# Optimization experiments

Hardware: AMD Instinct MI355X
Metric: run time of the kernel (lower is better)

## Reference

```python
import jax, jax.numpy as jnp
import numpy as np

N_QUBITS = 10
LAYERS = 4


def _ry(theta):
    c = jnp.cos(theta / 2).astype(jnp.complex64)
    s = jnp.sin(theta / 2).astype(jnp.complex64)
    return jnp.array([[c, -s], [s, c]], dtype=jnp.complex64)


def _rot(phi, theta, omega):
    # Rot = RZ(omega) RY(theta) RZ(phi)  (PennyLane convention)
    c = jnp.cos(theta / 2)
    s = jnp.sin(theta / 2)
    e_mm = jnp.exp(-0.5j * (phi + omega))
    e_pm = jnp.exp(0.5j * (phi - omega))
    e_mp = jnp.exp(-0.5j * (phi - omega))
    e_pp = jnp.exp(0.5j * (phi + omega))
    return jnp.array([[e_mm * c, -e_pm * s], [e_mp * s, e_pp * c]], dtype=jnp.complex64)


def _apply_1q(state, U, q):
    # state: (2,)*n complex; contract qubit axis q with 2x2 gate
    s = jnp.tensordot(U, state, axes=[[1], [q]])
    return jnp.moveaxis(s, 0, q)


def _apply_cnot(state, c, t):
    s = jnp.moveaxis(state, (c, t), (0, 1))
    s = jnp.stack([s[0], s[1, ::-1]], axis=0)
    return jnp.moveaxis(s, (0, 1), (c, t))


def _circuit(angles, weights):
    # angles: (n_qubits,) float32, weights: (layers, n_qubits, 3) float32
    n = N_QUBITS
    state = jnp.zeros((2 ** n,), dtype=jnp.complex64).at[0].set(1.0).reshape((2,) * n)
    for q in range(n):  # RY angle embedding
        state = _apply_1q(state, _ry(angles[q]), q)
    for l in range(LAYERS):  # strongly-entangling layers
        for q in range(n):
            state = _apply_1q(state, _rot(weights[l, q, 0], weights[l, q, 1], weights[l, q, 2]), q)
        for q in range(n):  # CNOT ring
            state = _apply_cnot(state, q, (q + 1) % n)
    probs = state.real ** 2 + state.imag ** 2  # (2,)*n
    zexp = []
    for q in range(n):
        p = probs.sum(axis=tuple(a for a in range(n) if a != q))
        zexp.append(p[0] - p[1])
    return jnp.stack(zexp)  # (n_qubits,)


def setup_inputs() -> dict:
    key = jax.random.key(0)
    ks = jax.random.split(key, 6)
    B, D = 8192, 784
    return {
        "x": jax.random.normal(ks[0], (B, D), dtype=jnp.float32),
        "Wp": jax.random.normal(ks[1], (N_QUBITS, D), dtype=jnp.float32) * (1.0 / np.sqrt(D)),
        "bp": jax.random.normal(ks[2], (N_QUBITS,), dtype=jnp.float32) * 0.01,
        "q_weights": jax.random.normal(ks[3], (LAYERS, N_QUBITS, 3), dtype=jnp.float32) * 0.01,
        "Wo": jax.random.normal(ks[4], (10, N_QUBITS), dtype=jnp.float32) * (1.0 / np.sqrt(N_QUBITS)),
        "bo": jax.random.normal(ks[5], (10,), dtype=jnp.float32) * 0.01,
    }


def reference(x, Wp, bp, q_weights, Wo, bo):
    # input projection + tanh
    h = jnp.tanh(x @ Wp.T + bp)  # (B, n_qubits)
    # batched quantum circuit (vmapped statevector simulation)
    q_out = jax.vmap(_circuit, in_axes=(0, None))(h, q_weights)  # (B, n_qubits)
    return q_out @ Wo.T + bo  # (B, 10) logits
```

## Files before the change

kernel.cpp:

```cpp
#include <hip/hip_runtime.h>

#define NQ      10
#define NLAYERS 4
#define D_IN    784
#define BLOCK   256

typedef __attribute__((ext_vector_type(2))) float f2;

__device__ __forceinline__ f2 swapc(f2 v) { return __builtin_shufflevector(v, v, 1, 0); }

template<int LB>
__device__ __forceinline__ float lx(float v) {
    if constexpr (LB == 1) {
        return __int_as_float(__builtin_amdgcn_update_dpp(
            0, __float_as_int(v), 0xB1, 0xF, 0xF, false));
    } else if constexpr (LB == 2) {
        return __int_as_float(__builtin_amdgcn_update_dpp(
            0, __float_as_int(v), 0x4E, 0xF, 0xF, false));
    } else if constexpr (LB == 8) {
        return __int_as_float(__builtin_amdgcn_update_dpp(
            0, __float_as_int(v), 0x128, 0xF, 0xF, false));
    } else {
        return __shfl_xor(v, LB, 64);
    }
}

template<int LB>
__device__ __forceinline__ f2 lx2(f2 v) {
    f2 r; r.x = lx<LB>(v.x); r.y = lx<LB>(v.y); return r;
}

template<int HALF>
__device__ __forceinline__ void plswap(f2 &d, f2 &s) {
    if constexpr (HALF == 32) {
        auto rx = __builtin_amdgcn_permlane32_swap(__float_as_int(d.x), __float_as_int(s.x), false, false);
        auto ry = __builtin_amdgcn_permlane32_swap(__float_as_int(d.y), __float_as_int(s.y), false, false);
        d.x = __int_as_float(rx[0]); s.x = __int_as_float(rx[1]);
        d.y = __int_as_float(ry[0]); s.y = __int_as_float(ry[1]);
    } else {
        auto rx = __builtin_amdgcn_permlane16_swap(__float_as_int(d.x), __float_as_int(s.x), false, false);
        auto ry = __builtin_amdgcn_permlane16_swap(__float_as_int(d.y), __float_as_int(s.y), false, false);
        d.x = __int_as_float(rx[0]); s.x = __int_as_float(rx[1]);
        d.y = __int_as_float(ry[0]); s.y = __int_as_float(ry[1]);
    }
}

template<int HALF>
__device__ __forceinline__ void rot_pl(f2 (&re)[8], f2 (&im)[8], float4 A, float4 B) {
#pragma unroll
    for (int a = 0; a < 8; a += 2) {
        f2 ur = re[a], vr = re[a + 1], ui = im[a], vi = im[a + 1];
        plswap<HALF>(ur, vr); plswap<HALF>(ui, vi);
        f2 nur = A.x*ur - A.y*ui + A.z*vr - A.w*vi;
        f2 nui = A.x*ui + A.y*ur + A.z*vi + A.w*vr;
        f2 nvr = B.x*ur - B.y*ui + B.z*vr - B.w*vi;
        f2 nvi = B.x*ui + B.y*ur + B.z*vi + B.w*vr;
        plswap<HALF>(nur, nvr); plswap<HALF>(nui, nvi);
        re[a] = nur; re[a + 1] = nvr; im[a] = nui; im[a + 1] = nvi;
    }
}

__device__ __forceinline__ void rot0_fused(f2 (&re)[8], f2 (&im)[8], float4 A, float4 B) {
    f2 CuAr, CuAi, CvAr, CvAi, CuBr, CuBi, CvBr, CvBi;
    CuAr.x = A.x; CuAr.y = A.z;   CuAi.x = A.y; CuAi.y = A.w;
    CvAr.x = A.z; CvAr.y = A.x;   CvAi.x = A.w; CvAi.y = A.y;
    CuBr.x = B.x; CuBr.y = B.z;   CuBi.x = B.y; CuBi.y = B.w;
    CvBr.x = B.z; CvBr.y = B.x;   CvBi.x = B.w; CvBi.y = B.y;
#pragma unroll
    for (int a = 0; a < 8; a += 2) {
        f2 ur = re[a], vr = re[a + 1], ui = im[a], vi = im[a + 1];
        plswap<32>(ur, vr); plswap<32>(ui, vi);
        f2 nur = CuAr*ur - CuAi*ui + CvAr*vr - CvAi*vi;
        f2 nui = CuAr*ui + CuAi*ur + CvAr*vi + CvAi*vr;
        f2 nvr = CuBr*ur - CuBi*ui + CvBr*vr - CvBi*vi;
        f2 nvi = CuBr*ui + CuBi*ur + CvBr*vi + CvBi*vr;
        plswap<32>(nur, nvr); plswap<32>(nui, nvi);
        re[a] = nur; re[a + 1] = nvr; im[a] = nui; im[a + 1] = nvi;
    }
}

template<int LB>
__device__ __forceinline__ void rot_lane(f2 (&re)[8], f2 (&im)[8], int lane, float4 A, float4 B) {
    const bool hi = (lane & LB) != 0;
    const float gdx = hi ? B.z : A.x, gdy = hi ? B.w : A.y;
    const float gox = hi ? B.x : A.z, goy = hi ? B.y : A.w;
#pragma unroll
    for (int a = 0; a < 8; a++) {
        f2 ore = lx2<LB>(re[a]);
        f2 oim = lx2<LB>(im[a]);
        f2 vr = re[a], vi = im[a];
        re[a] = gdx*vr - gdy*vi + gox*ore - goy*oim;
        im[a] = gdx*vi + gdy*vr + gox*oim + goy*ore;
    }
}

template<int MB>
__device__ __forceinline__ void rot_reg(f2 (&re)[8], f2 (&im)[8], float4 A, float4 B) {
#pragma unroll
    for (int a = 0; a < 8; a++) {
        if (!(a & MB)) {
            const int a1 = a | MB;
            f2 r0r = re[a], r0i = im[a], r1r = re[a1], r1i = im[a1];
            re[a]  = A.x*r0r - A.y*r0i + A.z*r1r - A.w*r1i;
            im[a]  = A.x*r0i + A.y*r0r + A.z*r1i + A.w*r1r;
            re[a1] = B.x*r0r - B.y*r0i + B.z*r1r - B.w*r1i;
            im[a1] = B.x*r0i + B.y*r0r + B.z*r1i + B.w*r1r;
        }
    }
}

__device__ __forceinline__ void rot_comp(f2 (&re)[8], f2 (&im)[8], float4 A, float4 B) {
    f2 K1, K2, K3, K4;
    K1.x = A.x; K1.y = B.z;   K2.x = -A.y; K2.y = -B.w;
    K3.x = A.z; K3.y = B.x;   K4.x = -A.w; K4.y = -B.y;
#pragma unroll
    for (int a = 0; a < 8; a++) {
        f2 sre = swapc(re[a]), sim = swapc(im[a]);
        f2 nre = K1*re[a] + K2*im[a] + K3*sre + K4*sim;
        f2 nim = K1*im[a] - K2*re[a] + K3*sim - K4*sre;
        re[a] = nre; im[a] = nim;
    }
}

__device__ __forceinline__ void swapf2(f2 &a, f2 &b) { f2 t = a; a = b; b = t; }

__device__ __forceinline__ void ring(f2 (&re)[8], f2 (&im)[8], int lane, int bidx) {
#pragma unroll
    for (int a = 0; a < 8; a++) {
        re[a].x = __int_as_float(__builtin_amdgcn_ds_bpermute(bidx, __float_as_int(re[a].x)));
        re[a].y = __int_as_float(__builtin_amdgcn_ds_bpermute(bidx, __float_as_int(re[a].y)));
        im[a].x = __int_as_float(__builtin_amdgcn_ds_bpermute(bidx, __float_as_int(im[a].x)));
        im[a].y = __int_as_float(__builtin_amdgcn_ds_bpermute(bidx, __float_as_int(im[a].y)));
    }
    const bool ctl = (lane & 1) != 0;
#pragma unroll
    for (int a = 0; a < 4; a++) {
        f2 A0 = re[a], A1 = re[a + 4], B0 = im[a], B1 = im[a + 4];
        f2 n0, n1, m0, m1;
        n0.x = ctl ? A1.x : A0.x;  n0.y = ctl ? A1.y : A0.y;
        n1.x = ctl ? A0.x : A1.x;  n1.y = ctl ? A0.y : A1.y;
        m0.x = ctl ? B1.x : B0.x;  m0.y = ctl ? B1.y : B0.y;
        m1.x = ctl ? B0.x : B1.x;  m1.y = ctl ? B0.y : B1.y;
        re[a] = n0; re[a + 4] = n1; im[a] = m0; im[a + 4] = m1;
    }
    swapf2(re[4], re[6]); swapf2(re[5], re[7]); swapf2(im[4], im[6]); swapf2(im[5], im[7]);
    swapf2(re[2], re[3]); swapf2(re[6], re[7]); swapf2(im[2], im[3]); swapf2(im[6], im[7]);
#pragma unroll
    for (int a = 1; a < 8; a += 2) { re[a] = swapc(re[a]); im[a] = swapc(im[a]); }
}

__global__ __launch_bounds__(BLOCK)
__attribute__((amdgpu_waves_per_eu(2, 8)))
void qnet_kernel(
    const float* __restrict__ x,
    const float* __restrict__ Wp,
    const float* __restrict__ bp,
    const float* __restrict__ qw,
    const float* __restrict__ Wo,
    const float* __restrict__ bo,
    float* __restrict__ out, int B)
{
    __shared__ __align__(16) float gates[NLAYERS * NQ * 8];

    const int tid  = threadIdx.x;
    const int lane = tid & 63;
    const int s    = blockIdx.x * (BLOCK / 64) + (tid >> 6);

    if (tid < NLAYERS * NQ) {
        float phi = qw[tid * 3 + 0];
        float th  = qw[tid * 3 + 1];
        float om  = qw[tid * 3 + 2];
        float sth, cth; sincosf(0.5f * th, &sth, &cth);
        float sap, cap; sincosf(0.5f * (phi + om), &sap, &cap);
        float sam, cam; sincosf(0.5f * (phi - om), &sam, &cam);
        float* g = &gates[tid * 8];
        g[0] =  cap * cth;  g[1] = -sap * cth;
        g[2] = -cam * sth;  g[3] = -sam * sth;
        g[4] =  cam * sth;  g[5] = -sam * sth;
        g[6] =  cap * cth;  g[7] =  sap * cth;
    }
    __syncthreads();
    if (s >= B) return;

    float acc[NQ];
#pragma unroll
    for (int q = 0; q < NQ; q++) acc[q] = 0.f;
    const float* xr = x + (size_t)s * D_IN;
#pragma unroll
    for (int it = 0; it < 3; it++) {
        const int d = (it * 64 + lane) * 4;
        float4 xv = *(const float4*)(xr + d);
#pragma unroll
        for (int q = 0; q < NQ; q++) {
            float4 wv = *(const float4*)(Wp + q * D_IN + d);
            acc[q] += xv.x * wv.x + xv.y * wv.y + xv.z * wv.z + xv.w * wv.w;
        }
    }
    if (lane < 4) {
        const int d = (192 + lane) * 4;
        float4 xv = *(const float4*)(xr + d);
#pragma unroll
        for (int q = 0; q < NQ; q++) {
            float4 wv = *(const float4*)(Wp + q * D_IN + d);
            acc[q] += xv.x * wv.x + xv.y * wv.y + xv.z * wv.z + xv.w * wv.w;
        }
    }
#pragma unroll
    for (int q = 0; q < NQ; q++) {
#pragma unroll
        for (int o = 1; o < 64; o <<= 1) acc[q] += __shfl_xor(acc[q], o, 64);
    }
    float myc = 1.f, mys = 0.f;
    if (lane < NQ) {
        float h = tanhf(acc[lane] + bp[lane]);
        sincosf(0.5f * h, &mys, &myc);
    }

    f2 re[8], im[8];
#pragma unroll
    for (int a = 0; a < 8; a++) { re[a].x = 0.f; re[a].y = 0.f; im[a].x = 0.f; im[a].y = 0.f; }
    if (lane == 0) re[0].x = 1.f;

    const int bidx = (lane ^ (lane >> 1)) << 2;

    {
        const float* gl = &gates[0];
#define MKMAT(Q) \
        float c0 = __shfl(myc, Q, 64), s0 = __shfl(mys, Q, 64); \
        float4 gA = *(const float4*)(gl + Q * 8); \
        float4 gB = *(const float4*)(gl + Q * 8 + 4); \
        float4 Am, Bm; \
        Am.x = gA.x * c0 + gA.z * s0;  Am.y = gA.y * c0 + gA.w * s0; \
        Am.z = gA.z * c0 - gA.x * s0;  Am.w = gA.w * c0 - gA.y * s0; \
        Bm.x = gB.x * c0 + gB.z * s0;  Bm.y = gB.y * c0 + gB.w * s0; \
        Bm.z = gB.z * c0 - gB.x * s0;  Bm.w = gB.w * c0 - gB.y * s0;
        { MKMAT(0); rot_pl<32>(re, im, Am, Bm); }
        { MKMAT(1); rot_pl<16>(re, im, Am, Bm); }
        { MKMAT(2); rot_lane<8>(re, im, lane, Am, Bm); }
        { MKMAT(3); rot_lane<4>(re, im, lane, Am, Bm); }
        { MKMAT(4); rot_lane<2>(re, im, lane, Am, Bm); }
        { MKMAT(5); rot_lane<1>(re, im, lane, Am, Bm); }
        { MKMAT(6); rot_reg<4>(re, im, Am, Bm); }
        { MKMAT(7); rot_reg<2>(re, im, Am, Bm); }
        { MKMAT(8); rot_reg<1>(re, im, Am, Bm); }
        { MKMAT(9); rot_comp(re, im, Am, Bm); }
#undef MKMAT
        ring(re, im, lane, bidx);
    }

    for (int l = 1; l < NLAYERS; l++) {
        const float* gl = &gates[l * NQ * 8];
#define GMAT(Q) *(const float4*)(gl + Q * 8), *(const float4*)(gl + Q * 8 + 4)
        rot0_fused(re, im, GMAT(0));
        rot_pl<16>(re, im, GMAT(1));
        rot_lane<8>(re, im, lane, GMAT(2));
        rot_lane<4>(re, im, lane, GMAT(3));
        rot_lane<2>(re, im, lane, GMAT(4));
        rot_lane<1>(re, im, lane, GMAT(5));
        rot_reg<4>(re, im, GMAT(6));
        rot_reg<2>(re, im, GMAT(7));
        rot_reg<1>(re, im, GMAT(8));
        rot_comp(re, im, GMAT(9));
#undef GMAT
        ring(re, im, lane, bidx);
    }

    f2 S2 = {0.f, 0.f}, z62 = {0.f, 0.f}, z72 = {0.f, 0.f}, z82 = {0.f, 0.f};
#pragma unroll
    for (int a = 0; a < 8; a++) {
        f2 p = re[a] * re[a] + im[a] * im[a];
        S2 += p;
        if (a & 4) z62 -= p; else z62 += p;
        if (a & 2) z72 -= p; else z72 += p;
        if (a & 1) z82 -= p; else z82 += p;
    }
    const float Ssum = S2.x + S2.y;
    const float Sdif = S2.x - S2.y;
    float zq[NQ];
    zq[0] = (lane & 32) ? -Sdif : Sdif;
    zq[1] = (lane & 16) ? -Ssum : Ssum;
    zq[2] = (lane &  8) ? -Ssum : Ssum;
    zq[3] = (lane &  4) ? -Ssum : Ssum;
    zq[4] = (lane &  2) ? -Ssum : Ssum;
    zq[5] = (lane &  1) ? -Ssum : Ssum;
    zq[6] = z62.x + z62.y;
    zq[7] = z72.x + z72.y;
    zq[8] = z82.x + z82.y;
    zq[9] = Sdif;
#pragma unroll
    for (int q = 0; q < NQ; q++) {
#pragma unroll
        for (int o = 1; o < 64; o <<= 1) zq[q] += __shfl_xor(zq[q], o, 64);
    }

    if (lane < NQ) {
        const float* wrow = Wo + lane * NQ;
        float o0 = bo[lane];
#pragma unroll
        for (int q = 0; q < NQ; q++) o0 += zq[q] * wrow[q];
        out[(size_t)s * NQ + lane] = o0;
    }
}

extern "C" void kernel_launch(void* const* d_in, const int* in_sizes, int n_in,
                              void* d_out, int out_size, void* d_ws, size_t ws_size,
                              hipStream_t stream) {
    const float* x  = (const float*)d_in[0];
    const float* Wp = (const float*)d_in[1];
    const float* bp = (const float*)d_in[2];
    const float* qw = (const float*)d_in[3];
    const float* Wo = (const float*)d_in[4];
    const float* bo = (const float*)d_in[5];
    float* out = (float*)d_out;

    const int B = in_sizes[0] / D_IN;
    const int spb = BLOCK / 64;
    const int blocks = (B + spb - 1) / spb;
    hipLaunchKernelGGL(qnet_kernel, dim3(blocks), dim3(BLOCK), 0, stream,
                       x, Wp, bp, qw, Wo, bo, out, B);
}
```

Measured before the change: 147.2 us.

## Factor Rot gates into per-layer diagonal RZ phases and real RY rotations

Each Rot gate is split into RZ·RY·RZ. All RZ phases in a layer are merged into one diagonal phase per amplitude, computed from per-lane sums and a precomputed table, and the RY parts become real 2x2 rotations that need far fewer FMAs. The angle-embedding layer is applied analytically as a product state instead of by simulated gates, and the final layer's trailing RZ is dropped because it does not change the probabilities. In exchange, per-lane sincos calls and extra complex multiplies are added for each diagonal application, and the setup of shared-memory tables becomes more involved.

```diff
diff --git a/kernel.cpp b/kernel.cpp
--- a/kernel.cpp
+++ b/kernel.cpp
@@ -5,8 +5,10 @@
 #define D_IN    784
 #define BLOCK   256
 
+
 typedef __attribute__((ext_vector_type(2))) float f2;
 
+__device__ __forceinline__ f2 sp(float v) { f2 r; r.x = v; r.y = v; return r; }
 __device__ __forceinline__ f2 swapc(f2 v) { return __builtin_shufflevector(v, v, 1, 0); }
 
 template<int LB>
@@ -46,79 +48,96 @@
 }
 
 template<int HALF>
-__device__ __forceinline__ void rot_pl(f2 (&re)[8], f2 (&im)[8], float4 A, float4 B) {
+__device__ __forceinline__ void ry_pl(f2 (&re)[8], f2 (&im)[8], float c, float s) {
 #pragma unroll
     for (int a = 0; a < 8; a += 2) {
         f2 ur = re[a], vr = re[a + 1], ui = im[a], vi = im[a + 1];
         plswap<HALF>(ur, vr); plswap<HALF>(ui, vi);
-        f2 nur = A.x*ur - A.y*ui + A.z*vr - A.w*vi;
-        f2 nui = A.x*ui + A.y*ur + A.z*vi + A.w*vr;
-        f2 nvr = B.x*ur - B.y*ui + B.z*vr - B.w*vi;
-        f2 nvi = B.x*ui + B.y*ur + B.z*vi + B.w*vr;
+        f2 nur = sp(c)*ur - sp(s)*vr;   f2 nui = sp(c)*ui - sp(s)*vi;
+        f2 nvr = sp(s)*ur + sp(c)*vr;   f2 nvi = sp(s)*ui + sp(c)*vi;
         plswap<HALF>(nur, nvr); plswap<HALF>(nui, nvi);
         re[a] = nur; re[a + 1] = nvr; im[a] = nui; im[a + 1] = nvi;
     }
 }
 
-__device__ __forceinline__ void rot0_fused(f2 (&re)[8], f2 (&im)[8], float4 A, float4 B) {
-    f2 CuAr, CuAi, CvAr, CvAi, CuBr, CuBi, CvBr, CvBi;
-    CuAr.x = A.x; CuAr.y = A.z;   CuAi.x = A.y; CuAi.y = A.w;
-    CvAr.x = A.z; CvAr.y = A.x;   CvAi.x = A.w; CvAi.y = A.y;
-    CuBr.x = B.x; CuBr.y = B.z;   CuBi.x = B.y; CuBi.y = B.w;
-    CvBr.x = B.z; CvBr.y = B.x;   CvBi.x = B.w; CvBi.y = B.y;
+__device__ __forceinline__ void ry0_fused(f2 (&re)[8], f2 (&im)[8], float c, float s) {
+    f2 K1, K2, K3, K4;
+    K1.x =  c; K1.y = -s;   K2.x = -s; K2.y =  c;
+    K3.x =  s; K3.y =  c;   K4.x =  c; K4.y =  s;
 #pragma unroll
     for (int a = 0; a < 8; a += 2) {
         f2 ur = re[a], vr = re[a + 1], ui = im[a], vi = im[a + 1];
         plswap<32>(ur, vr); plswap<32>(ui, vi);
-        f2 nur = CuAr*ur - CuAi*ui + CvAr*vr - CvAi*vi;
-        f2 nui = CuAr*ui + CuAi*ur + CvAr*vi + CvAi*vr;
-        f2 nvr = CuBr*ur - CuBi*ui + CvBr*vr - CvBi*vi;
-        f2 nvi = CuBr*ui + CuBi*ur + CvBr*vi + CvBi*vr;
+        f2 nur = K1*ur + K2*vr;   f2 nui = K1*ui + K2*vi;
+        f2 nvr = K3*ur + K4*vr;   f2 nvi = K3*ui + K4*vi;
         plswap<32>(nur, nvr); plswap<32>(nui, nvi);
         re[a] = nur; re[a + 1] = nvr; im[a] = nui; im[a + 1] = nvi;
     }
 }
 
 template<int LB>
-__device__ __forceinline__ void rot_lane(f2 (&re)[8], f2 (&im)[8], int lane, float4 A, float4 B) {
-    const bool hi = (lane & LB) != 0;
-    const float gdx = hi ? B.z : A.x, gdy = hi ? B.w : A.y;
-    const float gox = hi ? B.x : A.z, goy = hi ? B.y : A.w;
+__device__ __forceinline__ void ry_lane(f2 (&re)[8], f2 (&im)[8], int lane, float c, float s) {
+    const float o = (lane & LB) ? s : -s;
 #pragma unroll
     for (int a = 0; a < 8; a++) {
         f2 ore = lx2<LB>(re[a]);
         f2 oim = lx2<LB>(im[a]);
-        f2 vr = re[a], vi = im[a];
-        re[a] = gdx*vr - gdy*vi + gox*ore - goy*oim;
-        im[a] = gdx*vi + gdy*vr + gox*oim + goy*ore;
+        re[a] = sp(c)*re[a] + sp(o)*ore;
+        im[a] = sp(c)*im[a] + sp(o)*oim;
     }
 }
 
 template<int MB>
-__device__ __forceinline__ void rot_reg(f2 (&re)[8], f2 (&im)[8], float4 A, float4 B) {
+__device__ __forceinline__ void ry_reg(f2 (&re)[8], f2 (&im)[8], float c, float s) {
 #pragma unroll
     for (int a = 0; a < 8; a++) {
         if (!(a & MB)) {
             const int a1 = a | MB;
-            f2 r0r = re[a], r0i = im[a], r1r = re[a1], r1i = im[a1];
-            re[a]  = A.x*r0r - A.y*r0i + A.z*r1r - A.w*r1i;
-            im[a]  = A.x*r0i + A.y*r0r + A.z*r1i + A.w*r1r;
-            re[a1] = B.x*r0r - B.y*r0i + B.z*r1r - B.w*r1i;
-            im[a1] = B.x*r0i + B.y*r0r + B.z*r1i + B.w*r1r;
-        }
-    }
-}
-
-__device__ __forceinline__ void rot_comp(f2 (&re)[8], f2 (&im)[8], float4 A, float4 B) {
-    f2 K1, K2, K3, K4;
-    K1.x = A.x; K1.y = B.z;   K2.x = -A.y; K2.y = -B.w;
-    K3.x = A.z; K3.y = B.x;   K4.x = -A.w; K4.y = -B.y;
+            f2 r0 = re[a], r1 = re[a1], i0 = im[a], i1 = im[a1];
+            re[a]  = sp(c)*r0 - sp(s)*r1;   re[a1] = sp(s)*r0 + sp(c)*r1;
+            im[a]  = sp(c)*i0 - sp(s)*i1;   im[a1] = sp(s)*i0 + sp(c)*i1;
+        }
+    }
+}
+
+__device__ __forceinline__ void ry_comp(f2 (&re)[8], f2 (&im)[8], float c, float s) {
+    f2 Ks; Ks.x = -s; Ks.y = s;
 #pragma unroll
     for (int a = 0; a < 8; a++) {
         f2 sre = swapc(re[a]), sim = swapc(im[a]);
-        f2 nre = K1*re[a] + K2*im[a] + K3*sre + K4*sim;
-        f2 nim = K1*im[a] - K2*re[a] + K3*sim - K4*sre;
-        re[a] = nre; im[a] = nim;
+        re[a] = sp(c)*re[a] + Ks*sre;
+        im[a] = sp(c)*im[a] + Ks*sim;
+    }
+}
+
+template<bool XOR0>
+__device__ __forceinline__ void diag_apply(f2 (&re)[8], f2 (&im)[8], int lane,
+                                           const float* lz, const f2* DC, const f2* DS) {
+    float lp = 0.f;
+    lp += (lane & 16) ? lz[1] : -lz[1];
+    lp += (lane &  8) ? lz[2] : -lz[2];
+    lp += (lane &  4) ? lz[3] : -lz[3];
+    lp += (lane &  2) ? lz[4] : -lz[4];
+    lp += (lane &  1) ? lz[5] : -lz[5];
+    const float t0 = (lane & 32) ? lz[0] : -lz[0];
+    f2 cl, sl;
+    if constexpr (XOR0) {
+        float sa, ca, sb, cb;
+        sincosf(lp + t0, &sa, &ca);
+        sincosf(lp - t0, &sb, &cb);
+        cl.x = ca; cl.y = cb; sl.x = sa; sl.y = sb;
+    } else {
+        float sa, ca;
+        sincosf(lp + t0, &sa, &ca);
+        cl = sp(ca); sl = sp(sa);
+    }
+#pragma unroll
+    for (int a = 0; a < 8; a++) {
+        f2 cr = cl*DC[a] - sl*DS[a];
+        f2 ci = cl*DS[a] + sl*DC[a];
+        f2 nr = cr*re[a] - ci*im[a];
+        f2 ni = cr*im[a] + ci*re[a];
+        re[a] = nr; im[a] = ni;
     }
 }
 
@@ -160,24 +179,40 @@
     const float* __restrict__ bo,
     float* __restrict__ out, int B)
 {
-    __shared__ __align__(16) float gates[NLAYERS * NQ * 8];
+    __shared__ float ryt[NLAYERS * NQ * 2];
+    __shared__ float lzt[NLAYERS * 2 * 6];
+    __shared__ __align__(8) f2 dct[NLAYERS * 2 * 8];
+    __shared__ __align__(8) f2 dst[NLAYERS * 2 * 8];
 
     const int tid  = threadIdx.x;
     const int lane = tid & 63;
     const int s    = blockIdx.x * (BLOCK / 64) + (tid >> 6);
 
     if (tid < NLAYERS * NQ) {
-        float phi = qw[tid * 3 + 0];
-        float th  = qw[tid * 3 + 1];
-        float om  = qw[tid * 3 + 2];
-        float sth, cth; sincosf(0.5f * th, &sth, &cth);
-        float sap, cap; sincosf(0.5f * (phi + om), &sap, &cap);
-        float sam, cam; sincosf(0.5f * (phi - om), &sam, &cam);
-        float* g = &gates[tid * 8];
-        g[0] =  cap * cth;  g[1] = -sap * cth;
-        g[2] = -cam * sth;  g[3] = -sam * sth;
-        g[4] =  cam * sth;  g[5] = -sam * sth;
-        g[6] =  cap * cth;  g[7] =  sap * cth;
+        const int l = tid / NQ, q = tid % NQ;
+        float th = qw[tid * 3 + 1];
+        float sc, cc; sincosf(0.5f * th, &sc, &cc);
+        ryt[tid * 2] = cc; ryt[tid * 2 + 1] = sc;
+        if (q < 6) {
+            lzt[(l * 2 + 0) * 6 + q] = 0.5f * qw[tid * 3 + 0];
+            lzt[(l * 2 + 1) * 6 + q] = 0.5f * qw[tid * 3 + 2];
+        }
+    }
+    if (tid >= 64 && tid < 128) {
+        const int idx = tid - 64;
+        const int l = idx >> 4, t = (idx >> 3) & 1, a = idx & 7;
+        const float* ql = qw + (size_t)l * NQ * 3;
+        const int off = t ? 2 : 0;
+        const float p6 = 0.5f * ql[6 * 3 + off], p7 = 0.5f * ql[7 * 3 + off];
+        const float p8 = 0.5f * ql[8 * 3 + off], p9 = 0.5f * ql[9 * 3 + off];
+        const float base = ((a & 4) ? p6 : -p6) + ((a & 2) ? p7 : -p7) + ((a & 1) ? p8 : -p8);
+        float s0, c0, s1, c1;
+        sincosf(base - p9, &s0, &c0);
+        sincosf(base + p9, &s1, &c1);
+        f2 dc; dc.x = c0; dc.y = c1;
+        f2 ds; ds.x = s0; ds.y = s1;
+        dct[(l * 2 + t) * 8 + a] = dc;
+        dst[(l * 2 + t) * 8 + a] = ds;
     }
     __syncthreads();
     if (s >= B) return;
@@ -217,51 +252,61 @@
     }
 
     f2 re[8], im[8];
-#pragma unroll
-    for (int a = 0; a < 8; a++) { re[a].x = 0.f; re[a].y = 0.f; im[a].x = 0.f; im[a].y = 0.f; }
-    if (lane == 0) re[0].x = 1.f;
+    float lf = 1.f;
+    {
+        float cq, sq;
+#define SEL(Q, MASK) cq = __shfl(myc, Q, 64); sq = __shfl(mys, Q, 64); \
+                     lf *= (lane & MASK) ? sq : cq;
+        SEL(0, 32) SEL(1, 16) SEL(2, 8) SEL(3, 4) SEL(4, 2) SEL(5, 1)
+#undef SEL
+        const float c6 = __shfl(myc, 6, 64), s6 = __shfl(mys, 6, 64);
+        const float c7 = __shfl(myc, 7, 64), s7 = __shfl(mys, 7, 64);
+        const float c8 = __shfl(myc, 8, 64), s8 = __shfl(mys, 8, 64);
+        const float c9 = __shfl(myc, 9, 64), s9 = __shfl(mys, 9, 64);
+#pragma unroll
+        for (int a = 0; a < 8; a++) {
+            float t = ((a & 4) ? s6 : c6) * ((a & 2) ? s7 : c7) * ((a & 1) ? s8 : c8) * lf;
+            re[a].x = t * c9; re[a].y = t * s9;
+            im[a] = sp(0.f);
+        }
+    }
 
     const int bidx = (lane ^ (lane >> 1)) << 2;
 
     {
-        const float* gl = &gates[0];
-#define MKMAT(Q) \
-        float c0 = __shfl(myc, Q, 64), s0 = __shfl(mys, Q, 64); \
-        float4 gA = *(const float4*)(gl + Q * 8); \
-        float4 gB = *(const float4*)(gl + Q * 8 + 4); \
-        float4 Am, Bm; \
-        Am.x = gA.x * c0 + gA.z * s0;  Am.y = gA.y * c0 + gA.w * s0; \
-        Am.z = gA.z * c0 - gA.x * s0;  Am.w = gA.w * c0 - gA.y * s0; \
-        Bm.x = gB.x * c0 + gB.z * s0;  Bm.y = gB.y * c0 + gB.w * s0; \
-        Bm.z = gB.z * c0 - gB.x * s0;  Bm.w = gB.w * c0 - gB.y * s0;
-        { MKMAT(0); rot_pl<32>(re, im, Am, Bm); }
-        { MKMAT(1); rot_pl<16>(re, im, Am, Bm); }
-        { MKMAT(2); rot_lane<8>(re, im, lane, Am, Bm); }
-        { MKMAT(3); rot_lane<4>(re, im, lane, Am, Bm); }
-        { MKMAT(4); rot_lane<2>(re, im, lane, Am, Bm); }
-        { MKMAT(5); rot_lane<1>(re, im, lane, Am, Bm); }
-        { MKMAT(6); rot_reg<4>(re, im, Am, Bm); }
-        { MKMAT(7); rot_reg<2>(re, im, Am, Bm); }
-        { MKMAT(8); rot_reg<1>(re, im, Am, Bm); }
-        { MKMAT(9); rot_comp(re, im, Am, Bm); }
-#undef MKMAT
+        const float* rl = ryt;
+        diag_apply<false>(re, im, lane, lzt, dct, dst);
+        ry_pl<32>(re, im, rl[0], rl[1]);
+        ry_pl<16>(re, im, rl[2], rl[3]);
+        ry_lane<8>(re, im, lane, rl[4], rl[5]);
+        ry_lane<4>(re, im, lane, rl[6], rl[7]);
+        ry_lane<2>(re, im, lane, rl[8], rl[9]);
+        ry_lane<1>(re, im, lane, rl[10], rl[11]);
+        ry_reg<4>(re, im, rl[12], rl[13]);
+        ry_reg<2>(re, im, rl[14], rl[15]);
+        ry_reg<1>(re, im, rl[16], rl[17]);
+        ry_comp(re, im, rl[18], rl[19]);
+        diag_apply<false>(re, im, lane, lzt + 6, dct + 8, dst + 8);
         ring(re, im, lane, bidx);
     }
 
     for (int l = 1; l < NLAYERS; l++) {
-        const float* gl = &gates[l * NQ * 8];
-#define GMAT(Q) *(const float4*)(gl + Q * 8), *(const float4*)(gl + Q * 8 + 4)
-        rot0_fused(re, im, GMAT(0));
-        rot_pl<16>(re, im, GMAT(1));
-        rot_lane<8>(re, im, lane, GMAT(2));
-        rot_lane<4>(re, im, lane, GMAT(3));
-        rot_lane<2>(re, im, lane, GMAT(4));
-        rot_lane<1>(re, im, lane, GMAT(5));
-        rot_reg<4>(re, im, GMAT(6));
-        rot_reg<2>(re, im, GMAT(7));
-        rot_reg<1>(re, im, GMAT(8));
-        rot_comp(re, im, GMAT(9));
-#undef GMAT
+        const float* rl = ryt + l * NQ * 2;
+        diag_apply<true>(re, im, lane, lzt + (l * 2) * 6,
+                         dct + (l * 2) * 8, dst + (l * 2) * 8);
+        ry0_fused(re, im, rl[0], rl[1]);
+        ry_pl<16>(re, im, rl[2], rl[3]);
+        ry_lane<8>(re, im, lane, rl[4], rl[5]);
+        ry_lane<4>(re, im, lane, rl[6], rl[7]);
+        ry_lane<2>(re, im, lane, rl[8], rl[9]);
+        ry_lane<1>(re, im, lane, rl[10], rl[11]);
+        ry_reg<4>(re, im, rl[12], rl[13]);
+        ry_reg<2>(re, im, rl[14], rl[15]);
+        ry_reg<1>(re, im, rl[16], rl[17]);
+        ry_comp(re, im, rl[18], rl[19]);
+        if (l < NLAYERS - 1)
+            diag_apply<false>(re, im, lane, lzt + (l * 2 + 1) * 6,
+                              dct + (l * 2 + 1) * 8, dst + (l * 2 + 1) * 8);
         ring(re, im, lane, bidx);
     }
 
```

After: 139.6 us. 1.05x faster.
